# Kernel tuning notes

Measured on AMD Instinct MI355X. Metric: run time of the kernel, lower is better.

The kernel has to match this reference:

```python
import jax, jax.numpy as jnp
import numpy as np

N = 20000      # num nodes
E = 320000     # num edges (before self loops)
D = 512        # d_model
H = 4          # gnn_heads
C = 256        # gnn_hidden_dim (per-head out channels)
L = 4          # gnn_num_layers
B = 16         # number of graphs in batch
NEG_SLOPE = 0.2
LN_EPS = 1e-5


def setup_inputs() -> dict:
    key = jax.random.key(0)
    ks = jax.random.split(key, 10)
    s = 0.05
    return {
        "x": jax.random.normal(ks[0], (N, D), jnp.float32),
        "edge_index": jax.random.randint(ks[1], (2, E), 0, N, dtype=jnp.int32),
        "batch": jnp.sort(jax.random.randint(ks[2], (N,), 0, B, dtype=jnp.int32)),
        "W0": jax.random.normal(ks[3], (D, H * C), jnp.float32) * s,
        "W_rest": jax.random.normal(ks[4], (L - 1, H * C, H * C), jnp.float32) * s,
        "att_src": jax.random.normal(ks[5], (L, H, C), jnp.float32) * s,
        "att_dst": jax.random.normal(ks[6], (L, H, C), jnp.float32) * s,
        "conv_bias": jnp.zeros((L, H * C), jnp.float32),
        "proj_W": jax.random.normal(ks[7], (H * C, D), jnp.float32) * s,
        "proj_b": jnp.zeros((D,), jnp.float32),
        "ln_gamma": jnp.ones((D,), jnp.float32),
        "ln_beta": jnp.zeros((D,), jnp.float32),
    }


def _gat_layer(x, src, dst, W, a_src, a_dst, b):
    # x: [N, F_in] -> h: [N, H, C]
    h = (x @ W).reshape(N, H, C)
    alpha_src = jnp.einsum('nhc,hc->nh', h, a_src)   # [N, H]
    alpha_dst = jnp.einsum('nhc,hc->nh', h, a_dst)   # [N, H]
    e = jax.nn.leaky_relu(alpha_src[src] + alpha_dst[dst], NEG_SLOPE)  # [Etot, H]
    # per-destination softmax (every node has a self loop, so segments nonempty)
    m = jax.ops.segment_max(e, dst, num_segments=N)
    ex = jnp.exp(e - m[dst])
    denom = jax.ops.segment_sum(ex, dst, num_segments=N)
    alpha = ex / (denom[dst] + 1e-16)                # [Etot, H]
    out = jax.ops.segment_sum(alpha[:, :, None] * h[src], dst, num_segments=N)  # [N, H, C]
    return out.reshape(N, H * C) + b


def reference(x, edge_index, batch, W0, W_rest, att_src, att_dst, conv_bias,
              proj_W, proj_b, ln_gamma, ln_beta):
    # add self loops (PyG GATConv default)
    loop = jnp.arange(N, dtype=edge_index.dtype)
    src = jnp.concatenate([edge_index[0], loop])
    dst = jnp.concatenate([edge_index[1], loop])

    h = x
    for l in range(L):
        W = W0 if l == 0 else W_rest[l - 1]
        h = _gat_layer(h, src, dst, W, att_src[l], att_dst[l], conv_bias[l])
        h = jax.nn.relu(h)  # dropout: eval mode -> identity

    # global mean pool over nodes per graph
    sums = jax.ops.segment_sum(h, batch, num_segments=B)           # [B, H*C]
    counts = jax.ops.segment_sum(jnp.ones((N,), h.dtype), batch, num_segments=B)
    pooled = sums / jnp.maximum(counts, 1.0)[:, None]

    out = pooled @ proj_W + proj_b                                 # [B, D]
    mu = out.mean(-1, keepdims=True)
    var = ((out - mu) ** 2).mean(-1, keepdims=True)
    return (out - mu) / jnp.sqrt(var + LN_EPS) * ln_gamma + ln_beta
```

## Files before the change

kernel.cpp:

```cpp
#include <hip/hip_runtime.h>
#include <hip/hip_bf16.h>
#include <hip/hip_fp8.h>
#include <math.h>

#define Nn 20000
#define Ee 320000
#define Dd 512
#define Hh 4
#define Cc 256
#define Ll 4
#define Bb 16
#define HC 1024
#define ETOT (Ee + Nn)
#define NEG_SLOPE 0.2f
#define LN_EPS 1e-5f
#define NBLK ((Nn + 255) / 256)

typedef __attribute__((ext_vector_type(8))) __bf16 bf16x8;
typedef __attribute__((ext_vector_type(4))) __bf16 bf16x4;
typedef __attribute__((ext_vector_type(4))) float f32x4;
typedef __attribute__((ext_vector_type(2))) float f32x2;

__device__ __forceinline__ f32x4 fp8x4_to_f32(unsigned int v) {
#if __has_builtin(__builtin_amdgcn_cvt_pk_f32_fp8)
    f32x2 lo = __builtin_amdgcn_cvt_pk_f32_fp8((int)v, false);
    f32x2 hi = __builtin_amdgcn_cvt_pk_f32_fp8((int)v, true);
    f32x4 r; r[0] = lo[0]; r[1] = lo[1]; r[2] = hi[0]; r[3] = hi[1];
    return r;
#else
    f32x4 r;
    #pragma unroll
    for (int i = 0; i < 4; ++i) {
        __hip_fp8_e4m3 q; q.__x = (v >> (8 * i)) & 0xff;
        r[i] = (float)q;
    }
    return r;
#endif
}

__device__ __forceinline__ unsigned char f32_to_fp8(float f) {
    return __hip_fp8_e4m3(f).__x;
}


__device__ __forceinline__ void decode_edge(const int* ei, int e, int& s, int& d) {
    if (e < Ee) { s = ei[e]; d = ei[Ee + e]; }
    else        { s = e - Ee; d = e - Ee; }
}

__global__ void count_deg_kernel(const int* __restrict__ ei, int* __restrict__ deg) {
    int e = blockIdx.x * blockDim.x + threadIdx.x;
    if (e >= ETOT) return;
    int s, d; decode_edge(ei, e, s, d);
    atomicAdd(&deg[d], 1);
}

__global__ void scan1_kernel(const int* __restrict__ deg, int* __restrict__ tmp,
                             int* __restrict__ bsum) {
    __shared__ int sd[256];
    int tid = threadIdx.x;
    int i = blockIdx.x * 256 + tid;
    sd[tid] = (i < Nn) ? deg[i] : 0;
    __syncthreads();
    for (int off = 1; off < 256; off <<= 1) {
        int t = (tid >= off) ? sd[tid - off] : 0;
        __syncthreads();
        sd[tid] += t;
        __syncthreads();
    }
    if (i < Nn) tmp[i] = sd[tid];
    if (tid == 255) bsum[blockIdx.x] = sd[255];
}

__global__ void scan2_kernel(int* __restrict__ bsum) {
    __shared__ int sd[256];
    int tid = threadIdx.x;
    sd[tid] = (tid < NBLK) ? bsum[tid] : 0;
    __syncthreads();
    for (int off = 1; off < 256; off <<= 1) {
        int t = (tid >= off) ? sd[tid - off] : 0;
        __syncthreads();
        sd[tid] += t;
        __syncthreads();
    }
    if (tid < NBLK) bsum[tid] = sd[tid];
}

__global__ void scan3_kernel(const int* __restrict__ tmp, const int* __restrict__ bsum,
                             const int* __restrict__ deg,
                             int* __restrict__ row_ptr, int* __restrict__ cursor) {
    int i = blockIdx.x * 256 + threadIdx.x;
    if (i >= Nn) return;
    int boff = (blockIdx.x == 0) ? 0 : bsum[blockIdx.x - 1];
    int incl = tmp[i] + boff;
    row_ptr[i + 1] = incl;
    cursor[i] = incl - deg[i];
    if (i == 0) row_ptr[0] = 0;
}

__global__ void scatter_kernel(const int* __restrict__ ei, int* __restrict__ cursor,
                               int* __restrict__ csr_src) {
    int e = blockIdx.x * blockDim.x + threadIdx.x;
    if (e >= ETOT) return;
    int s, d; decode_edge(ei, e, s, d);
    int pos = atomicAdd(&cursor[d], 1);
    csr_src[pos] = s;
}


__global__ void cast_kernel(const float* __restrict__ in, __bf16* __restrict__ out, int n4) {
    int i = blockIdx.x * blockDim.x + threadIdx.x;
    if (i >= n4) return;
    f32x4 v = ((const f32x4*)in)[i];
    bf16x4 o;
    #pragma unroll
    for (int k = 0; k < 4; ++k) o[k] = (__bf16)v[k];
    ((bf16x4*)out)[i] = o;
}

__global__ void transpose_cast_kernel(const float* __restrict__ W, __bf16* __restrict__ WT,
                                      int K, int N) {
    __shared__ float tile[32][33];
    int n0 = blockIdx.x * 32, k0 = blockIdx.y * 32;
    for (int i = threadIdx.y; i < 32; i += 8)
        tile[i][threadIdx.x] = W[(size_t)(k0 + i) * N + n0 + threadIdx.x];
    __syncthreads();
    for (int i = threadIdx.y; i < 32; i += 8)
        WT[(size_t)(n0 + i) * K + k0 + threadIdx.x] = (__bf16)tile[threadIdx.x][i];
}


__global__ __launch_bounds__(256) void wtilde_kernel(const float* __restrict__ W0,
                                                     const float* __restrict__ W_rest,
                                                     const float* __restrict__ att_src,
                                                     const float* __restrict__ att_dst,
                                                     __bf16* __restrict__ wt) {
    int g = blockIdx.x * 4 + (threadIdx.x >> 6);
    int lane = threadIdx.x & 63;
    if (g >= 3584) return;
    int l, k;
    const float* row;
    if (g < 512) { l = 0; k = g; row = W0 + (size_t)k * HC; }
    else {
        int gg = g - 512; l = 1 + (gg >> 10); k = gg & 1023;
        row = W_rest + (size_t)(l - 1) * HC * HC + (size_t)k * HC;
    }
    const float* as = att_src + l * HC;
    const float* ad = att_dst + l * HC;
    int c0 = lane * 16;
    int head = lane >> 4;
    float s = 0.f, d = 0.f;
    #pragma unroll
    for (int c = 0; c < 16; ++c) {
        float w = row[c0 + c];
        s += w * as[c0 + c];
        d += w * ad[c0 + c];
    }
    #pragma unroll
    for (int off = 1; off < 16; off <<= 1) {
        s += __shfl_xor(s, off);
        d += __shfl_xor(d, off);
    }
    if ((lane & 15) == 0) {
        wt[((size_t)l * 1024 + k) * 8 + head * 2]     = (__bf16)s;
        wt[((size_t)l * 1024 + k) * 8 + head * 2 + 1] = (__bf16)d;
    }
}


__global__ __launch_bounds__(256) void alpha_gemv_kernel(const __bf16* __restrict__ A,
                                                         const __bf16* __restrict__ wt_l,
                                                         float* __restrict__ asrc,
                                                         float* __restrict__ adst, int K) {
    int n = blockIdx.x * 4 + (threadIdx.x >> 6);
    int lane = threadIdx.x & 63;
    if (n >= Nn) return;
    float acc[8] = {};
    for (int k0 = lane * 8; k0 < K; k0 += 512) {
        bf16x8 av = *(const bf16x8*)(A + (size_t)n * K + k0);
        #pragma unroll
        for (int kk = 0; kk < 8; ++kk) {
            float af = (float)av[kk];
            bf16x8 wv = *(const bf16x8*)(wt_l + (size_t)(k0 + kk) * 8);
            #pragma unroll
            for (int j = 0; j < 8; ++j) acc[j] += af * (float)wv[j];
        }
    }
    #pragma unroll
    for (int off = 32; off > 0; off >>= 1)
        #pragma unroll
        for (int j = 0; j < 8; ++j) acc[j] += __shfl_down(acc[j], off);
    if (lane == 0) {
        #pragma unroll
        for (int h = 0; h < 4; ++h) {
            asrc[n * 4 + h] = acc[h * 2];
            adst[n * 4 + h] = acc[h * 2 + 1];
        }
    }
}


__device__ __forceinline__ void async16(const __bf16* g, __bf16* l) {
    __builtin_amdgcn_global_load_lds((const __attribute__((address_space(1))) void*)g,
                                     (__attribute__((address_space(3))) void*)l,
                                     16, 0, 0);
}

__global__ __launch_bounds__(256) void mfma_gemm_kernel(
    const __bf16* __restrict__ A,
    const __bf16* __restrict__ BT,
    unsigned char* __restrict__ C8,
    int M, int K)
{
    int lin = blockIdx.y * 8 + blockIdx.x;
    int rblk = (lin >> 6) * 8 + (lin & 7);
    int cblk = (lin >> 3) & 7;
    int rowBase = rblk * 128, colBase = cblk * 128;
    if (rowBase >= M) return;

    __shared__ __bf16 As[2][128 * 32];
    __shared__ __bf16 Bs[2][128 * 32];
    int tid = threadIdx.x;
    int wave = tid >> 6, lane = tid & 63;
    int m16 = lane & 15, quad = lane >> 4;
    int waveRow = (wave >> 1) * 64, waveCol = (wave & 1) * 64;

    f32x4 acc[4][4] = {};

    int srow = wave * 32 + (lane >> 2);
    int gch0 = (lane & 3) ^ ((srow >> 1) & 3);
    int gch1 = (lane & 3) ^ (((srow + 16) >> 1) & 3);
    int gr0 = rowBase + srow;       if (gr0 >= M) gr0 = M - 1;
    int gr1 = rowBase + srow + 16;  if (gr1 >= M) gr1 = M - 1;
    int ldsOff = srow * 32 + (lane & 3) * 8;

    for (int k0 = 0; k0 < K; k0 += 64) {
        #pragma unroll
        for (int p = 0; p < 2; ++p) {
            int kp = k0 + p * 32;
            async16(A + (size_t)gr0 * K + kp + gch0 * 8, &As[p][ldsOff]);
            async16(A + (size_t)gr1 * K + kp + gch1 * 8, &As[p][ldsOff + 16 * 32]);
            async16(BT + (size_t)(colBase + srow) * K + kp + gch0 * 8, &Bs[p][ldsOff]);
            async16(BT + (size_t)(colBase + srow + 16) * K + kp + gch1 * 8, &Bs[p][ldsOff + 16 * 32]);
        }
        __syncthreads();
        #pragma unroll
        for (int p = 0; p < 2; ++p) {
            bf16x8 af[4], bfr[4];
            #pragma unroll
            for (int i = 0; i < 4; ++i) {
                int row = waveRow + i * 16 + m16;
                af[i] = *(const bf16x8*)&As[p][row * 32 + (quad ^ ((row >> 1) & 3)) * 8];
                int col = waveCol + i * 16 + m16;
                bfr[i] = *(const bf16x8*)&Bs[p][col * 32 + (quad ^ ((col >> 1) & 3)) * 8];
            }
            #pragma unroll
            for (int i = 0; i < 4; ++i)
                #pragma unroll
                for (int j = 0; j < 4; ++j)
                    acc[i][j] = __builtin_amdgcn_mfma_f32_16x16x32_bf16(af[i], bfr[j], acc[i][j], 0, 0, 0);
        }
        __syncthreads();
    }

    #pragma unroll
    for (int i = 0; i < 4; ++i) {
        int r0 = rowBase + waveRow + i * 16 + quad * 4;
        #pragma unroll
        for (int r = 0; r < 4; ++r) {
            int row = r0 + r;
            if (row < M) {
                #pragma unroll
                for (int j = 0; j < 4; ++j)
                    C8[(size_t)row * HC + colBase + waveCol + j * 16 + m16] =
                        f32_to_fp8(acc[i][j][r]);
            }
        }
    }
}


__global__ __launch_bounds__(256) void ew_kernel(const float* __restrict__ asrc,
                                                 const float* __restrict__ adst,
                                                 const int* __restrict__ row_ptr,
                                                 const int* __restrict__ csr_src,
                                                 float* __restrict__ ewT,
                                                 float* __restrict__ dinv) {
    int w = threadIdx.x >> 6, lane = threadIdx.x & 63;
    int n = blockIdx.x * 4 + w;
    if (n >= Nn) return;
    int start = row_ptr[n], end = row_ptr[n + 1];
    f32x4 ad = ((const f32x4*)adst)[n];
    f32x4 d = {0.f, 0.f, 0.f, 0.f};
    for (int e = start + lane; e < end; e += 64) {
        int s = csr_src[e];
        f32x4 as = ((const f32x4*)asrc)[s];
        #pragma unroll
        for (int k = 0; k < 4; ++k) {
            float z = as[k] + ad[k];
            z = (z > 0.f) ? z : NEG_SLOPE * z;
            float ex = __expf(z);
            ewT[(size_t)k * ETOT + e] = ex;
            d[k] += ex;
        }
    }
    #pragma unroll
    for (int off = 32; off > 0; off >>= 1) {
        #pragma unroll
        for (int k = 0; k < 4; ++k) d[k] += __shfl_down(d[k], off);
    }
    if (lane == 0) {
        f32x4 iv;
        #pragma unroll
        for (int k = 0; k < 4; ++k) iv[k] = 1.f / (d[k] + 1e-16f);
        ((f32x4*)dinv)[n] = iv;
    }
}


__global__ __launch_bounds__(256) void agg_slice_kernel(
    const unsigned char* __restrict__ h8,
    const float* __restrict__ ewT,
    const float* __restrict__ dinv,
    const int* __restrict__ row_ptr,
    const int* __restrict__ csr_src,
    const float* __restrict__ bias_l,
    __bf16* __restrict__ outb)
{
    int slice = blockIdx.x;
    int head = slice >> 1;
    int tid = threadIdx.x;
    int nslot = tid >> 4;
    int ch = tid & 15;
    int n = blockIdx.y * 16 + nslot;

    __shared__ int   csr_sh[512];
    __shared__ float ew_sh[512];
    __shared__ int   rp_sh[17];

    if (tid < 17) rp_sh[tid] = row_ptr[blockIdx.y * 16 + tid];
    __syncthreads();
    int blk_lo = rp_sh[0], blk_hi = rp_sh[16];
    int start = rp_sh[nslot], end = rp_sh[nslot + 1];

    const unsigned char* hs = h8 + slice * 128 + ch * 8;
    const float* ewh = ewT + (size_t)head * ETOT;
    float acc[8] = {};

    for (int c0 = blk_lo; c0 < blk_hi; c0 += 512) {
        int c1 = min(c0 + 512, blk_hi);
        int cnt = c1 - c0;
        for (int i = tid; i < cnt; i += 256) {
            csr_sh[i] = csr_src[c0 + i];
            ew_sh[i]  = ewh[c0 + i];
        }
        __syncthreads();
        int lo = max(start, c0), hi = min(end, c1);
        int e = lo;
        for (; e + 1 < hi; e += 2) {
            int s0 = csr_sh[e - c0], s1 = csr_sh[e + 1 - c0];
            float w0 = ew_sh[e - c0], w1 = ew_sh[e + 1 - c0];
            uint2 u0 = *(const uint2*)(hs + (size_t)s0 * HC);
            uint2 u1 = *(const uint2*)(hs + (size_t)s1 * HC);
            f32x4 a0 = fp8x4_to_f32(u0.x), b0 = fp8x4_to_f32(u0.y);
            f32x4 a1 = fp8x4_to_f32(u1.x), b1 = fp8x4_to_f32(u1.y);
            #pragma unroll
            for (int k = 0; k < 4; ++k) {
                acc[k]     += w0 * a0[k];
                acc[k + 4] += w0 * b0[k];
                acc[k]     += w1 * a1[k];
                acc[k + 4] += w1 * b1[k];
            }
        }
        if (e < hi) {
            int s0 = csr_sh[e - c0];
            float w0 = ew_sh[e - c0];
            uint2 u0 = *(const uint2*)(hs + (size_t)s0 * HC);
            f32x4 a0 = fp8x4_to_f32(u0.x), b0 = fp8x4_to_f32(u0.y);
            #pragma unroll
            for (int k = 0; k < 4; ++k) {
                acc[k]     += w0 * a0[k];
                acc[k + 4] += w0 * b0[k];
            }
        }
        __syncthreads();
    }

    float inv = dinv[n * 4 + head];
    bf16x8 o;
    #pragma unroll
    for (int k = 0; k < 8; ++k)
        o[k] = (__bf16)fmaxf(acc[k] * inv + bias_l[slice * 128 + ch * 8 + k], 0.f);
    *(bf16x8*)(outb + (size_t)n * HC + slice * 128 + ch * 8) = o;
}


__device__ __forceinline__ int lower_bound_batch(const int* __restrict__ batch, int val) {
    int lo = 0, hi = Nn;
    while (lo < hi) { int mid = (lo + hi) >> 1; if (batch[mid] < val) lo = mid + 1; else hi = mid; }
    return lo;
}

__global__ void pool_kernel(const __bf16* __restrict__ h2b, const int* __restrict__ batch,
                            float* __restrict__ pooled) {
    int b = blockIdx.x, part = blockIdx.y;
    int tid = threadIdx.x;
    int start = lower_bound_batch(batch, b);
    int end   = lower_bound_batch(batch, b + 1);
    int len = end - start;
    int chunk = (len + 7) / 8;
    int s0 = start + part * chunk;
    int s1 = min(s0 + chunk, end);
    float acc[4] = {0.f, 0.f, 0.f, 0.f};
    for (int n = s0; n < s1; ++n) {
        bf16x4 v = ((const bf16x4*)(h2b + (size_t)n * HC))[tid];
        #pragma unroll
        for (int k = 0; k < 4; ++k) acc[k] += (float)v[k];
    }
    #pragma unroll
    for (int k = 0; k < 4; ++k)
        atomicAdd(&pooled[b * HC + tid * 4 + k], acc[k]);
}


__global__ __launch_bounds__(512) void proj_partial_kernel(const float* __restrict__ pooled,
                                                           const int* __restrict__ batch,
                                                           const float* __restrict__ projW,
                                                           float* __restrict__ projOut) {
    int b = blockIdx.x, part = blockIdx.y;
    int d = threadIdx.x;
    int start = lower_bound_batch(batch, b);
    int end   = lower_bound_batch(batch, b + 1);
    float inv = 1.0f / fmaxf((float)(end - start), 1.0f);
    float acc = 0.f;
    int k0 = part * 128;
    for (int k = k0; k < k0 + 128; ++k)
        acc += pooled[b * HC + k] * projW[(size_t)k * Dd + d];
    atomicAdd(&projOut[b * Dd + d], acc * inv);
}

__global__ __launch_bounds__(512) void ln_kernel(const float* __restrict__ projOut,
                                                 const float* __restrict__ projb,
                                                 const float* __restrict__ gamma,
                                                 const float* __restrict__ beta,
                                                 float* __restrict__ out) {
    int b = blockIdx.x;
    int d = threadIdx.x;
    __shared__ float red[512];
    float o = projOut[b * Dd + d] + projb[d];
    red[d] = o;
    __syncthreads();
    for (int off = 256; off > 0; off >>= 1) {
        if (d < off) red[d] += red[d + off];
        __syncthreads();
    }
    float mu = red[0] / (float)Dd;
    __syncthreads();
    float df = o - mu;
    red[d] = df * df;
    __syncthreads();
    for (int off = 256; off > 0; off >>= 1) {
        if (d < off) red[d] += red[d + off];
        __syncthreads();
    }
    float var = red[0] / (float)Dd;
    out[b * Dd + d] = df / sqrtf(var + LN_EPS) * gamma[d] + beta[d];
}


extern "C" void kernel_launch(void* const* d_in, const int* in_sizes, int n_in,
                              void* d_out, int out_size, void* d_ws, size_t ws_size,
                              hipStream_t stream) {
    const float* x         = (const float*)d_in[0];
    const int*   ei        = (const int*)d_in[1];
    const int*   batch     = (const int*)d_in[2];
    const float* W0        = (const float*)d_in[3];
    const float* W_rest    = (const float*)d_in[4];
    const float* att_src   = (const float*)d_in[5];
    const float* att_dst   = (const float*)d_in[6];
    const float* conv_bias = (const float*)d_in[7];
    const float* proj_W    = (const float*)d_in[8];
    const float* proj_b    = (const float*)d_in[9];
    const float* ln_gamma  = (const float*)d_in[10];
    const float* ln_beta   = (const float*)d_in[11];
    float* out = (float*)d_out;

    char* ws = (char*)d_ws;
    size_t off = 0;
    auto alloc = [&](size_t bytes) {
        void* p = ws + off;
        off = (off + bytes + 255) & ~(size_t)255;
        return p;
    };
    unsigned char* h8 = (unsigned char*)alloc((size_t)Nn * HC);
    __bf16* h2b     = (__bf16*)alloc((size_t)Nn * HC * 2);
    __bf16* xb      = (__bf16*)alloc((size_t)Nn * Dd * 2);
    __bf16* W0T     = (__bf16*)alloc((size_t)HC * Dd * 2);
    __bf16* WrT     = (__bf16*)alloc((size_t)3 * HC * HC * 2);
    __bf16* wt      = (__bf16*)alloc((size_t)4 * 1024 * 8 * 2);
    float*  asrc    = (float*)alloc((size_t)Nn * Hh * 4);
    float*  adst    = (float*)alloc((size_t)Nn * Hh * 4);
    float*  ewT     = (float*)alloc((size_t)Hh * ETOT * 4);
    float*  dinv    = (float*)alloc((size_t)Nn * Hh * 4);
    int*    deg     = (int*)alloc((size_t)Nn * 4);
    int*    tmp     = (int*)alloc((size_t)Nn * 4);
    int*    bsum    = (int*)alloc((size_t)256 * 4);
    int*    row_ptr = (int*)alloc((size_t)(Nn + 1) * 4);
    int*    cursor  = (int*)alloc((size_t)Nn * 4);
    int*    csr_src = (int*)alloc((size_t)ETOT * 4);
    float*  pooled  = (float*)alloc((size_t)Bb * HC * 4);
    float*  projOut = (float*)alloc((size_t)Bb * Dd * 4);
    (void)ws_size; (void)in_sizes; (void)n_in; (void)out_size;

    hipMemsetAsync(deg, 0, (size_t)Nn * 4, stream);
    count_deg_kernel<<<(ETOT + 255) / 256, 256, 0, stream>>>(ei, deg);
    scan1_kernel<<<NBLK, 256, 0, stream>>>(deg, tmp, bsum);
    scan2_kernel<<<1, 256, 0, stream>>>(bsum);
    scan3_kernel<<<NBLK, 256, 0, stream>>>(tmp, bsum, deg, row_ptr, cursor);
    scatter_kernel<<<(ETOT + 255) / 256, 256, 0, stream>>>(ei, cursor, csr_src);

    cast_kernel<<<(Nn * Dd / 4 + 255) / 256, 256, 0, stream>>>(x, xb, Nn * Dd / 4);
    transpose_cast_kernel<<<dim3(HC / 32, Dd / 32), dim3(32, 8), 0, stream>>>(W0, W0T, Dd, HC);
    for (int l = 0; l < 3; ++l)
        transpose_cast_kernel<<<dim3(HC / 32, HC / 32), dim3(32, 8), 0, stream>>>(
            W_rest + (size_t)l * HC * HC, WrT + (size_t)l * HC * HC, HC, HC);
    wtilde_kernel<<<(3584 + 3) / 4, 256, 0, stream>>>(W0, W_rest, att_src, att_dst, wt);

    dim3 gemm_grid(8, 160);
    for (int l = 0; l < Ll; ++l) {
        const __bf16* Afeat = (l == 0) ? xb : h2b;
        int K = (l == 0) ? Dd : HC;
        const __bf16* BT = (l == 0) ? W0T : (WrT + (size_t)(l - 1) * HC * HC);
        alpha_gemv_kernel<<<(Nn + 3) / 4, 256, 0, stream>>>(
            Afeat, wt + (size_t)l * 1024 * 8, asrc, adst, K);
        mfma_gemm_kernel<<<gemm_grid, 256, 0, stream>>>(Afeat, BT, h8, Nn, K);
        ew_kernel<<<(Nn + 3) / 4, 256, 0, stream>>>(asrc, adst, row_ptr, csr_src, ewT, dinv);
        agg_slice_kernel<<<dim3(8, Nn / 16), 256, 0, stream>>>(
            h8, ewT, dinv, row_ptr, csr_src, conv_bias + l * HC, h2b);
    }

    hipMemsetAsync(pooled, 0, (size_t)Bb * HC * 4, stream);
    hipMemsetAsync(projOut, 0, (size_t)Bb * Dd * 4, stream);
    pool_kernel<<<dim3(Bb, 8), 256, 0, stream>>>(h2b, batch, pooled);
    proj_partial_kernel<<<dim3(Bb, 8), 512, 0, stream>>>(pooled, batch, proj_W, projOut);
    ln_kernel<<<Bb, 512, 0, stream>>>(projOut, proj_b, ln_gamma, ln_beta, out);
}
```

Before: 780.5 us.

## Fuse next-layer attention logit projection into aggregation epilogue

```diff
diff --git a/kernel.cpp b/kernel.cpp
--- a/kernel.cpp
+++ b/kernel.cpp
@@ -121,6 +121,8 @@
 __global__ void transpose_cast_kernel(const float* __restrict__ W, __bf16* __restrict__ WT,
                                       int K, int N) {
     __shared__ float tile[32][33];
+    W  += (size_t)blockIdx.z * K * N;
+    WT += (size_t)blockIdx.z * K * N;
     int n0 = blockIdx.x * 32, k0 = blockIdx.y * 32;
     for (int i = threadIdx.y; i < 32; i += 8)
         tile[i][threadIdx.x] = W[(size_t)(k0 + i) * N + n0 + threadIdx.x];
@@ -196,6 +198,27 @@
             asrc[n * 4 + h] = acc[h * 2];
             adst[n * 4 + h] = acc[h * 2 + 1];
         }
+    }
+}
+
+
+__global__ void alpha_reduce_kernel(const float* __restrict__ aprt,
+                                    float* __restrict__ asrc, float* __restrict__ adst) {
+    int n = blockIdx.x * 256 + threadIdx.x;
+    if (n >= Nn) return;
+    float s[8] = {};
+    #pragma unroll
+    for (int sl = 0; sl < 8; ++sl) {
+        const float* p = aprt + ((size_t)sl * Nn + n) * 8;
+        f32x4 a = *(const f32x4*)p;
+        f32x4 b = *(const f32x4*)(p + 4);
+        #pragma unroll
+        for (int j = 0; j < 4; ++j) { s[j] += a[j]; s[j + 4] += b[j]; }
+    }
+    #pragma unroll
+    for (int h = 0; h < 4; ++h) {
+        asrc[n * 4 + h] = s[h * 2];
+        adst[n * 4 + h] = s[h * 2 + 1];
     }
 }
 
@@ -325,7 +348,9 @@
     const int* __restrict__ row_ptr,
     const int* __restrict__ csr_src,
     const float* __restrict__ bias_l,
-    __bf16* __restrict__ outb)
+    __bf16* __restrict__ outb,
+    const __bf16* __restrict__ wt_next,
+    float* __restrict__ aprt)
 {
     int slice = blockIdx.x;
     int head = slice >> 1;
@@ -357,22 +382,28 @@
         __syncthreads();
         int lo = max(start, c0), hi = min(end, c1);
         int e = lo;
-        for (; e + 1 < hi; e += 2) {
+        for (; e + 3 < hi; e += 4) {
             int s0 = csr_sh[e - c0], s1 = csr_sh[e + 1 - c0];
+            int s2 = csr_sh[e + 2 - c0], s3 = csr_sh[e + 3 - c0];
             float w0 = ew_sh[e - c0], w1 = ew_sh[e + 1 - c0];
+            float w2 = ew_sh[e + 2 - c0], w3 = ew_sh[e + 3 - c0];
             uint2 u0 = *(const uint2*)(hs + (size_t)s0 * HC);
             uint2 u1 = *(const uint2*)(hs + (size_t)s1 * HC);
+            uint2 u2 = *(const uint2*)(hs + (size_t)s2 * HC);
+            uint2 u3 = *(const uint2*)(hs + (size_t)s3 * HC);
             f32x4 a0 = fp8x4_to_f32(u0.x), b0 = fp8x4_to_f32(u0.y);
             f32x4 a1 = fp8x4_to_f32(u1.x), b1 = fp8x4_to_f32(u1.y);
+            f32x4 a2 = fp8x4_to_f32(u2.x), b2 = fp8x4_to_f32(u2.y);
+            f32x4 a3 = fp8x4_to_f32(u3.x), b3 = fp8x4_to_f32(u3.y);
             #pragma unroll
             for (int k = 0; k < 4; ++k) {
-                acc[k]     += w0 * a0[k];
-                acc[k + 4] += w0 * b0[k];
-                acc[k]     += w1 * a1[k];
-                acc[k + 4] += w1 * b1[k];
+                acc[k]     += w0 * a0[k] + w1 * a1[k];
+                acc[k + 4] += w0 * b0[k] + w1 * b1[k];
+                acc[k]     += w2 * a2[k] + w3 * a3[k];
+                acc[k + 4] += w2 * b2[k] + w3 * b3[k];
             }
         }
-        if (e < hi) {
+        for (; e < hi; ++e) {
             int s0 = csr_sh[e - c0];
             float w0 = ew_sh[e - c0];
             uint2 u0 = *(const uint2*)(hs + (size_t)s0 * HC);
@@ -392,6 +423,26 @@
     for (int k = 0; k < 8; ++k)
         o[k] = (__bf16)fmaxf(acc[k] * inv + bias_l[slice * 128 + ch * 8 + k], 0.f);
     *(bf16x8*)(outb + (size_t)n * HC + slice * 128 + ch * 8) = o;
+
+    if (wt_next) {
+        float p[8] = {};
+        #pragma unroll
+        for (int k = 0; k < 8; ++k) {
+            float vk = (float)o[k];
+            bf16x8 wv = *(const bf16x8*)(wt_next + (size_t)(slice * 128 + ch * 8 + k) * 8);
+            #pragma unroll
+            for (int j = 0; j < 8; ++j) p[j] += vk * (float)wv[j];
+        }
+        #pragma unroll
+        for (int off = 1; off < 16; off <<= 1)
+            #pragma unroll
+            for (int j = 0; j < 8; ++j) p[j] += __shfl_xor(p[j], off);
+        if (ch == 0) {
+            #pragma unroll
+            for (int j = 0; j < 8; ++j)
+                aprt[((size_t)slice * Nn + n) * 8 + j] = p[j];
+        }
+    }
 }
 
 
@@ -402,7 +453,7 @@
 }
 
 __global__ void pool_kernel(const __bf16* __restrict__ h2b, const int* __restrict__ batch,
-                            float* __restrict__ pooled) {
+                            float* __restrict__ pooledP) {
     int b = blockIdx.x, part = blockIdx.y;
     int tid = threadIdx.x;
     int start = lower_bound_batch(batch, b);
@@ -419,27 +470,35 @@
     }
     #pragma unroll
     for (int k = 0; k < 4; ++k)
-        atomicAdd(&pooled[b * HC + tid * 4 + k], acc[k]);
-}
-
-
-__global__ __launch_bounds__(512) void proj_partial_kernel(const float* __restrict__ pooled,
+        pooledP[((size_t)part * Bb + b) * HC + tid * 4 + k] = acc[k];
+}
+
+
+__global__ __launch_bounds__(512) void proj_partial_kernel(const float* __restrict__ pooledP,
                                                            const int* __restrict__ batch,
                                                            const float* __restrict__ projW,
-                                                           float* __restrict__ projOut) {
+                                                           float* __restrict__ projP) {
     int b = blockIdx.x, part = blockIdx.y;
     int d = threadIdx.x;
+    __shared__ float psum[HC];
     int start = lower_bound_batch(batch, b);
     int end   = lower_bound_batch(batch, b + 1);
     float inv = 1.0f / fmaxf((float)(end - start), 1.0f);
+    for (int k = d; k < HC; k += 512) {
+        float s = 0.f;
+        #pragma unroll
+        for (int p = 0; p < 8; ++p) s += pooledP[((size_t)p * Bb + b) * HC + k];
+        psum[k] = s * inv;
+    }
+    __syncthreads();
     float acc = 0.f;
     int k0 = part * 128;
     for (int k = k0; k < k0 + 128; ++k)
-        acc += pooled[b * HC + k] * projW[(size_t)k * Dd + d];
-    atomicAdd(&projOut[b * Dd + d], acc * inv);
-}
-
-__global__ __launch_bounds__(512) void ln_kernel(const float* __restrict__ projOut,
+        acc += psum[k] * projW[(size_t)k * Dd + d];
+    projP[((size_t)part * Bb + b) * Dd + d] = acc;
+}
+
+__global__ __launch_bounds__(512) void ln_kernel(const float* __restrict__ projP,
                                                  const float* __restrict__ projb,
                                                  const float* __restrict__ gamma,
                                                  const float* __restrict__ beta,
@@ -447,7 +506,9 @@
     int b = blockIdx.x;
     int d = threadIdx.x;
     __shared__ float red[512];
-    float o = projOut[b * Dd + d] + projb[d];
+    float o = projb[d];
+    #pragma unroll
+    for (int p = 0; p < 8; ++p) o += projP[((size_t)p * Bb + b) * Dd + d];
     red[d] = o;
     __syncthreads();
     for (int off = 256; off > 0; off >>= 1) {
@@ -500,6 +561,7 @@
     __bf16* wt      = (__bf16*)alloc((size_t)4 * 1024 * 8 * 2);
     float*  asrc    = (float*)alloc((size_t)Nn * Hh * 4);
     float*  adst    = (float*)alloc((size_t)Nn * Hh * 4);
+    float*  aprt    = (float*)alloc((size_t)8 * Nn * 8 * 4);
     float*  ewT     = (float*)alloc((size_t)Hh * ETOT * 4);
     float*  dinv    = (float*)alloc((size_t)Nn * Hh * 4);
     int*    deg     = (int*)alloc((size_t)Nn * 4);
@@ -508,8 +570,8 @@
     int*    row_ptr = (int*)alloc((size_t)(Nn + 1) * 4);
     int*    cursor  = (int*)alloc((size_t)Nn * 4);
     int*    csr_src = (int*)alloc((size_t)ETOT * 4);
-    float*  pooled  = (float*)alloc((size_t)Bb * HC * 4);
-    float*  projOut = (float*)alloc((size_t)Bb * Dd * 4);
+    float*  pooledP = (float*)alloc((size_t)8 * Bb * HC * 4);
+    float*  projP   = (float*)alloc((size_t)8 * Bb * Dd * 4);
     (void)ws_size; (void)in_sizes; (void)n_in; (void)out_size;
 
     hipMemsetAsync(deg, 0, (size_t)Nn * 4, stream);
@@ -520,28 +582,26 @@
     scatter_kernel<<<(ETOT + 255) / 256, 256, 0, stream>>>(ei, cursor, csr_src);
 
     cast_kernel<<<(Nn * Dd / 4 + 255) / 256, 256, 0, stream>>>(x, xb, Nn * Dd / 4);
-    transpose_cast_kernel<<<dim3(HC / 32, Dd / 32), dim3(32, 8), 0, stream>>>(W0, W0T, Dd, HC);
-    for (int l = 0; l < 3; ++l)
-        transpose_cast_kernel<<<dim3(HC / 32, HC / 32), dim3(32, 8), 0, stream>>>(
-            W_rest + (size_t)l * HC * HC, WrT + (size_t)l * HC * HC, HC, HC);
+    transpose_cast_kernel<<<dim3(HC / 32, Dd / 32, 1), dim3(32, 8), 0, stream>>>(W0, W0T, Dd, HC);
+    transpose_cast_kernel<<<dim3(HC / 32, HC / 32, 3), dim3(32, 8), 0, stream>>>(W_rest, WrT, HC, HC);
     wtilde_kernel<<<(3584 + 3) / 4, 256, 0, stream>>>(W0, W_rest, att_src, att_dst, wt);
+    alpha_gemv_kernel<<<(Nn + 3) / 4, 256, 0, stream>>>(xb, wt, asrc, adst, Dd);
 
     dim3 gemm_grid(8, 160);
     for (int l = 0; l < Ll; ++l) {
         const __bf16* Afeat = (l == 0) ? xb : h2b;
         int K = (l == 0) ? Dd : HC;
         const __bf16* BT = (l == 0) ? W0T : (WrT + (size_t)(l - 1) * HC * HC);
-        alpha_gemv_kernel<<<(Nn + 3) / 4, 256, 0, stream>>>(
-            Afeat, wt + (size_t)l * 1024 * 8, asrc, adst, K);
+        if (l > 0)
+            alpha_reduce_kernel<<<NBLK, 256, 0, stream>>>(aprt, asrc, adst);
         mfma_gemm_kernel<<<gemm_grid, 256, 0, stream>>>(Afeat, BT, h8, Nn, K);
         ew_kernel<<<(Nn + 3) / 4, 256, 0, stream>>>(asrc, adst, row_ptr, csr_src, ewT, dinv);
+        const __bf16* wt_next = (l < Ll - 1) ? (wt + (size_t)(l + 1) * 1024 * 8) : nullptr;
         agg_slice_kernel<<<dim3(8, Nn / 16), 256, 0, stream>>>(
-            h8, ewT, dinv, row_ptr, csr_src, conv_bias + l * HC, h2b);
-    }
-
-    hipMemsetAsync(pooled, 0, (size_t)Bb * HC * 4, stream);
-    hipMemsetAsync(projOut, 0, (size_t)Bb * Dd * 4, stream);
-    pool_kernel<<<dim3(Bb, 8), 256, 0, stream>>>(h2b, batch, pooled);
-    proj_partial_kernel<<<dim3(Bb, 8), 512, 0, stream>>>(pooled, batch, proj_W, projOut);
-    ln_kernel<<<Bb, 512, 0, stream>>>(projOut, proj_b, ln_gamma, ln_beta, out);
-}
+            h8, ewT, dinv, row_ptr, csr_src, conv_bias + l * HC, h2b, wt_next, aprt);
+    }
+
+    pool_kernel<<<dim3(Bb, 8), 256, 0, stream>>>(h2b, batch, pooledP);
+    proj_partial_kernel<<<dim3(Bb, 8), 512, 0, stream>>>(pooledP, batch, proj_W, projP);
+    ln_kernel<<<Bb, 512, 0, stream>>>(projP, proj_b, ln_gamma, ln_beta, out);
+}
```

New measurement: 780.3 us. Within noise of the previous version (-0.0%).
